# Kernel optimization log

Measured on AMD Instinct MI355X. Metric: run time of the kernel, lower is better.

The kernel has to match this reference:

```python
import jax, jax.numpy as jnp
import numpy as np
from jax import lax

DIM = 256          # C
D_INNER = 512      # expand * dim
D_STATE = 16       # N
DT_RANK = 32       # ceil(d_inner / 16)
K_CONV = 4


def setup_inputs() -> dict:
    key = jax.random.key(0)
    ks = jax.random.split(key, 20)
    B, C, H, W = 2, DIM, 64, 64
    Di, N, R = D_INNER, D_STATE, DT_RANK
    s = 0.02
    inp = {
        "decoder_feat": jax.random.normal(ks[0], (B, C, H, W), jnp.float32),
        "encoder_feat": jax.random.normal(ks[1], (B, C, H, W), jnp.float32),
        # CrossMambaFusion params
        "dec_w": jax.random.normal(ks[2], (C, 2 * Di), jnp.float32) * s,
        "dec_b": jnp.zeros((2 * Di,), jnp.float32),
        "enc_w": jax.random.normal(ks[3], (C, Di), jnp.float32) * s,
        "enc_b": jnp.zeros((Di,), jnp.float32),
        "out_w": jax.random.normal(ks[4], (Di, C), jnp.float32) * s,
        "out_b": jnp.zeros((C,), jnp.float32),
        "ln_g": jnp.ones((C,), jnp.float32),
        "ln_b": jnp.zeros((C,), jnp.float32),
        # Mamba block params (inner dim = Di, expand=1.0)
        "in_w": jax.random.normal(ks[5], (Di, 2 * Di), jnp.float32) * s,
        "in_b": jnp.zeros((2 * Di,), jnp.float32),
        "conv_w": jax.random.normal(ks[6], (Di, 1, K_CONV), jnp.float32) * 0.1,
        "conv_b": jnp.zeros((Di,), jnp.float32),
        "x_proj_w": jax.random.normal(ks[7], (Di, R + 2 * N), jnp.float32) * s,
        "dt_w": jax.random.normal(ks[8], (R, Di), jnp.float32) * 0.1,
        "dt_b": jax.random.uniform(ks[9], (Di,), jnp.float32, -4.0, -2.0),  # small dt after softplus
        "A_log": jnp.log(jnp.tile(jnp.arange(1, N + 1, dtype=jnp.float32)[None, :], (Di, 1))),
        "D_param": jnp.ones((Di,), jnp.float32),
        "m_out_w": jax.random.normal(ks[10], (Di, Di), jnp.float32) * s,
        "m_out_b": jnp.zeros((Di,), jnp.float32),
    }
    return inp


def _mamba(x, in_w, in_b, conv_w, conv_b, x_proj_w, dt_w, dt_b, A_log, D_param, m_out_w, m_out_b):
    # x: (B, L, Di)
    Bsz, L, Di = x.shape
    N, R = D_STATE, DT_RANK
    xz = x @ in_w + in_b                      # (B, L, 2*Di)
    xm, z = jnp.split(xz, 2, axis=-1)
    # causal depthwise conv over the sequence axis
    xc = jnp.swapaxes(xm, 1, 2)               # (B, Di, L)
    xc = lax.conv_general_dilated(
        xc, conv_w, window_strides=(1,), padding=[(K_CONV - 1, 0)],
        dimension_numbers=("NCH", "OIH", "NCH"), feature_group_count=Di)
    xc = xc + conv_b[None, :, None]
    u = jax.nn.silu(jnp.swapaxes(xc, 1, 2))   # (B, L, Di)
    x_dbl = u @ x_proj_w                      # (B, L, R+2N)
    dt = jax.nn.softplus(x_dbl[..., :R] @ dt_w + dt_b)   # (B, L, Di)
    Bm = x_dbl[..., R:R + N]                  # (B, L, N)
    Cm = x_dbl[..., R + N:]                   # (B, L, N)
    A = -jnp.exp(A_log)                       # (Di, N)

    def step(h, t):
        dt_t, u_t, B_t, C_t = t               # (B,Di),(B,Di),(B,N),(B,N)
        dA = jnp.exp(dt_t[..., None] * A)     # (B, Di, N)
        h = h * dA + (dt_t * u_t)[..., None] * B_t[:, None, :]
        y = jnp.einsum("bdn,bn->bd", h, C_t)
        return h, y

    h0 = jnp.zeros((Bsz, Di, N), x.dtype)
    _, ys = lax.scan(step, h0, (jnp.swapaxes(dt, 0, 1), jnp.swapaxes(u, 0, 1),
                                jnp.swapaxes(Bm, 0, 1), jnp.swapaxes(Cm, 0, 1)))
    y = jnp.swapaxes(ys, 0, 1) + u * D_param  # skip connection via D
    y = y * jax.nn.silu(z)
    return y @ m_out_w + m_out_b


def reference(decoder_feat, encoder_feat, dec_w, dec_b, enc_w, enc_b, out_w, out_b,
              ln_g, ln_b, in_w, in_b, conv_w, conv_b, x_proj_w, dt_w, dt_b,
              A_log, D_param, m_out_w, m_out_b):
    B, C, H, W = decoder_feat.shape
    Di = D_INNER
    dec = jnp.transpose(decoder_feat, (0, 2, 3, 1)).reshape(B, H * W, C)
    enc = jnp.transpose(encoder_feat, (0, 2, 3, 1)).reshape(B, H * W, C)
    dec_proj = dec @ dec_w + dec_b
    dec_x, dec_gate = dec_proj[..., :Di], dec_proj[..., Di:]
    enc_p = enc @ enc_w + enc_b
    combined = dec_x * jax.nn.sigmoid(enc_p) + enc_p          # (B, L, Di)
    processed = _mamba(combined, in_w, in_b, conv_w, conv_b, x_proj_w,
                       dt_w, dt_b, A_log, D_param, m_out_w, m_out_b)
    out = (processed * jax.nn.sigmoid(dec_gate)) @ out_w + out_b
    res = out + dec
    mu = jnp.mean(res, axis=-1, keepdims=True)
    var = jnp.mean(jnp.square(res - mu), axis=-1, keepdims=True)
    res = (res - mu) * lax.rsqrt(var + 1e-5) * ln_g + ln_b
    return jnp.transpose(res.reshape(B, H, W, C), (0, 3, 1, 2))
```

## Files before the change

kernel.cpp:

```cpp
#include <hip/hip_runtime.h>
#include <hip/hip_bf16.h>

typedef __bf16 bf16x8_t __attribute__((ext_vector_type(8)));
typedef float f32x4_t __attribute__((ext_vector_type(4)));

__device__ __forceinline__ float sigmoidf_(float x) { return 1.0f / (1.0f + __expf(-x)); }
__device__ __forceinline__ float siluf_(float x) { return x * sigmoidf_(x); }
__device__ __forceinline__ float softplusf_(float x) {
    return fmaxf(x, 0.0f) + log1pf(__expf(-fabsf(x)));
}
__device__ __forceinline__ float b2f(ushort u) { return __uint_as_float(((unsigned)u) << 16); }
__device__ __forceinline__ ushort f2b(float f) {
    return (ushort)__bfloat16_as_ushort(__float2bfloat16(f));
}

__global__ __launch_bounds__(256) void k_prep(
    const float* __restrict__ dec_w, const float* __restrict__ enc_w,
    const float* __restrict__ in_w, const float* __restrict__ m_out_w,
    const float* __restrict__ out_w, const float* __restrict__ x_proj_w,
    const float* __restrict__ dt_w,
    const float* __restrict__ dec, const float* __restrict__ enc,
    __hip_bfloat16* __restrict__ dec_wT, __hip_bfloat16* __restrict__ enc_wT,
    __hip_bfloat16* __restrict__ in_wT, __hip_bfloat16* __restrict__ m_out_wT,
    __hip_bfloat16* __restrict__ out_wT, __hip_bfloat16* __restrict__ xpwT,
    __hip_bfloat16* __restrict__ dtwT,
    __hip_bfloat16* __restrict__ decL, __hip_bfloat16* __restrict__ encL)
{
    __shared__ float tile[64][65];
    if (blockIdx.x < 5312) {
        int gid = blockIdx.x * 256 + threadIdx.x;
        const float* src; __hip_bfloat16* dst; int lk, N, idx;
        if (gid < 262144)       { src = dec_w;    dst = dec_wT;   lk = 8; N = 1024; idx = gid; }
        else if (gid < 393216)  { src = enc_w;    dst = enc_wT;   lk = 8; N = 512;  idx = gid - 262144; }
        else if (gid < 917504)  { src = in_w;     dst = in_wT;    lk = 9; N = 1024; idx = gid - 393216; }
        else if (gid < 1179648) { src = m_out_w;  dst = m_out_wT; lk = 9; N = 512;  idx = gid - 917504; }
        else if (gid < 1310720) { src = out_w;    dst = out_wT;   lk = 9; N = 256;  idx = gid - 1179648; }
        else if (gid < 1343488) { src = x_proj_w; dst = xpwT;     lk = 9; N = 64;   idx = gid - 1310720; }
        else                    { src = dt_w;     dst = dtwT;     lk = 5; N = 512;  idx = gid - 1343488; }
        int K = 1 << lk;
        int n = idx >> lk, k = idx & (K - 1);
        dst[idx] = __float2bfloat16(src[(size_t)k * N + n]);
        return;
    }
    const int bid = blockIdx.x - 5312;
    const int t = threadIdx.x;
    const int ct = bid & 3;
    const int lt = (bid >> 2) & 63;
    const int sel = bid >> 8;
    const int b = sel & 1, ten = sel >> 1;
    const float* src = ten ? enc : dec;
    __hip_bfloat16* dst = ten ? encL : decL;
    const size_t ibase = (size_t)b * 256 * 4096 + (size_t)(ct * 64) * 4096 + (size_t)lt * 64;
#pragma unroll
    for (int i = 0; i < 16; ++i) {
        int c = i * 4 + (t >> 6), l = t & 63;
        tile[c][l] = src[ibase + (size_t)c * 4096 + l];
    }
    __syncthreads();
    const size_t obase = ((size_t)b * 4096 + (size_t)lt * 64) * 256 + ct * 64;
#pragma unroll
    for (int i = 0; i < 16; ++i) {
        int l = i * 4 + (t >> 6), c = t & 63;
        dst[obase + (size_t)l * 256 + c] = __float2bfloat16(tile[c][l]);
    }
}

template <int EPI, int K>
__global__ __launch_bounds__(256) void bgemm(
    const __hip_bfloat16* __restrict__ A, const __hip_bfloat16* __restrict__ Bt,
    const float* __restrict__ bias, void* __restrict__ out0,
    void* __restrict__ out1, const void* __restrict__ extra)
{
    __shared__ ushort At[128 * 32];
    __shared__ ushort Bl[128 * 32];
    const int tid = threadIdx.x;
    const int wave = tid >> 6, lane = tid & 63;
    const int n0 = blockIdx.x * 128, m0 = blockIdx.y * 128;
    const int wm = (wave >> 1) * 64, wn = (wave & 1) * 64;
    f32x4_t acc[4][4] = {};
    const int fr = lane & 15, fq = (lane >> 4) * 8;

    for (int k0 = 0; k0 < K; k0 += 32) {
#pragma unroll
        for (int q = 0; q < 2; ++q) {
            int idx = q * 256 + tid;
            int row = idx >> 2, ch = (idx & 3) * 8;
            uint4 va = *(const uint4*)&A[(size_t)(m0 + row) * K + k0 + ch];
            uint4 vb = *(const uint4*)&Bt[(size_t)(n0 + row) * K + k0 + ch];
            *(uint4*)&At[row * 32 + ch] = va;
            *(uint4*)&Bl[row * 32 + ch] = vb;
        }
        __syncthreads();
        bf16x8_t af[4], bf[4];
#pragma unroll
        for (int i = 0; i < 4; ++i) {
            af[i] = *(bf16x8_t*)&At[(wm + i * 16 + fr) * 32 + fq];
            bf[i] = *(bf16x8_t*)&Bl[(wn + i * 16 + fr) * 32 + fq];
        }
#pragma unroll
        for (int i = 0; i < 4; ++i)
#pragma unroll
            for (int j = 0; j < 4; ++j)
                acc[i][j] = __builtin_amdgcn_mfma_f32_16x16x32_bf16(af[i], bf[j], acc[i][j], 0, 0, 0);
        __syncthreads();
    }

    const int col = lane & 15, rbase = (lane >> 4) * 4;
#pragma unroll
    for (int i = 0; i < 4; ++i) {
#pragma unroll
        for (int j = 0; j < 4; ++j) {
#pragma unroll
            for (int r = 0; r < 4; ++r) {
                int m = m0 + wm + i * 16 + rbase + r;
                int n = n0 + wn + j * 16 + col;
                float v = acc[i][j][r] + bias[n];
                if (EPI == 0) {
                    ((__hip_bfloat16*)out0)[(size_t)m * 512 + n] = __float2bfloat16(v);
                } else if (EPI == 1) {
                    if (n < 512) {
                        float ep = __bfloat162float(((const __hip_bfloat16*)extra)[(size_t)m * 512 + n]);
                        ((__hip_bfloat16*)out0)[(size_t)m * 512 + n] =
                            __float2bfloat16(fmaf(v, sigmoidf_(ep), ep));
                    } else {
                        ((__hip_bfloat16*)out1)[(size_t)m * 512 + (n - 512)] =
                            __float2bfloat16(sigmoidf_(v));
                    }
                } else if (EPI == 2) {
                    if (n < 512)
                        ((__hip_bfloat16*)out0)[(size_t)m * 512 + n] = __float2bfloat16(v);
                    else
                        ((__hip_bfloat16*)out1)[(size_t)m * 512 + (n - 512)] =
                            __float2bfloat16(siluf_(v));
                } else {
                    float g = __bfloat162float(((const __hip_bfloat16*)extra)[(size_t)m * 512 + n]);
                    ((__hip_bfloat16*)out0)[(size_t)m * 512 + n] = __float2bfloat16(v * g);
                }
            }
        }
    }
}

#define CHUNK 16
#define NCHUNK 256

__global__ __launch_bounds__(512) void k_conv_scan(
    const __hip_bfloat16* __restrict__ xm, const float* __restrict__ conv_w,
    const float* __restrict__ conv_b, const __hip_bfloat16* __restrict__ xpwT,
    const __hip_bfloat16* __restrict__ dtwT, const float* __restrict__ dt_b,
    const float* __restrict__ A_log,
    __hip_bfloat16* __restrict__ u_out, float* __restrict__ Bm,
    float* __restrict__ Cm, __hip_bfloat16* __restrict__ dt_out,
    float* __restrict__ hpart, float* __restrict__ dtsums)
{
    __shared__ __align__(16) ushort us_dts[CHUNK][512 + 8];
    __shared__ __align__(16) ushort adt[CHUNK][32 + 8];
    __shared__ float BsL[CHUNK * 16];
    const int tid = threadIdx.x;
    const int wave = tid >> 6, lane = tid & 63;
    const int bl0 = blockIdx.x * CHUNK;
    const int l0 = bl0 & 4095;
    const int b = blockIdx.x >> 8;
    const int chunk = blockIdx.x & (NCHUNK - 1);
    const int fr = lane & 15, fq = (lane >> 4) * 8;
    const int col = lane & 15, rbase = (lane >> 4) * 4;

    float uarr[CHUNK];
    {
        const int d = tid;
        const float cw0 = conv_w[d * 4], cw1 = conv_w[d * 4 + 1];
        const float cw2 = conv_w[d * 4 + 2], cw3 = conv_w[d * 4 + 3];
        const float cb = conv_b[d];
        const ushort* xs = (const ushort*)xm;
        float x0 = (l0 >= 3) ? b2f(xs[(size_t)(bl0 - 3) * 512 + d]) : 0.f;
        float x1 = (l0 >= 2) ? b2f(xs[(size_t)(bl0 - 2) * 512 + d]) : 0.f;
        float x2 = (l0 >= 1) ? b2f(xs[(size_t)(bl0 - 1) * 512 + d]) : 0.f;
#pragma unroll
        for (int t = 0; t < CHUNK; ++t) {
            float x3 = b2f(xs[(size_t)(bl0 + t) * 512 + d]);
            float a = cb;
            a = fmaf(cw0, x0, a);
            a = fmaf(cw1, x1, a);
            a = fmaf(cw2, x2, a);
            a = fmaf(cw3, x3, a);
            float uv = siluf_(a);
            uarr[t] = uv;
            ushort ub = f2b(uv);
            us_dts[t][d] = ub;
            ((ushort*)u_out)[(size_t)(bl0 + t) * 512 + d] = ub;
            x0 = x1; x1 = x2; x2 = x3;
        }
    }
    __syncthreads();

    if (wave < 4) {
        const int n0w = wave * 16;
        f32x4_t acc = {};
        const __hip_bfloat16* bp = xpwT + (size_t)(n0w + fr) * 512;
#pragma unroll
        for (int k0 = 0; k0 < 512; k0 += 32) {
            bf16x8_t af = *(bf16x8_t*)&us_dts[fr][k0 + fq];
            bf16x8_t bf = *(const bf16x8_t*)&bp[k0 + fq];
            acc = __builtin_amdgcn_mfma_f32_16x16x32_bf16(af, bf, acc, 0, 0, 0);
        }
#pragma unroll
        for (int r = 0; r < 4; ++r) {
            int m = rbase + r;
            int n = n0w + col;
            float v = acc[r];
            if (n < 32) {
                adt[m][n] = f2b(v);
            } else if (n < 48) {
                BsL[m * 16 + (n - 32)] = v;
                Bm[(size_t)(bl0 + m) * 16 + (n - 32)] = v;
            } else {
                Cm[(size_t)(bl0 + m) * 16 + (n - 48)] = v;
            }
        }
    }
    __syncthreads();

    {
        bf16x8_t af = *(bf16x8_t*)&adt[fr][fq];
#pragma unroll
        for (int t = 0; t < 4; ++t) {
            int nt = wave * 4 + t;
            bf16x8_t bf = *(const bf16x8_t*)&dtwT[(size_t)(nt * 16 + fr) * 32 + fq];
            f32x4_t acc = {};
            acc = __builtin_amdgcn_mfma_f32_16x16x32_bf16(af, bf, acc, 0, 0, 0);
#pragma unroll
            for (int r = 0; r < 4; ++r) {
                int m = rbase + r;
                int n = nt * 16 + col;
                ushort dv = f2b(softplusf_(acc[r] + dt_b[n]));
                us_dts[m][n] = dv;
                ((ushort*)dt_out)[(size_t)(bl0 + m) * 512 + n] = dv;
            }
        }
    }
    __syncthreads();

    {
        const int d = tid;
        float Av[16];
#pragma unroll
        for (int n = 0; n < 16; n += 4) {
            float4 al = *(const float4*)&A_log[d * 16 + n];
            Av[n + 0] = -__expf(al.x);
            Av[n + 1] = -__expf(al.y);
            Av[n + 2] = -__expf(al.z);
            Av[n + 3] = -__expf(al.w);
        }
        float h[16] = {};
        float dtsum = 0.f;
#pragma unroll
        for (int t = 0; t < CHUNK; ++t) {
            float dtv = b2f(us_dts[t][d]);
            float dtu = dtv * uarr[t];
            dtsum += dtv;
            const float* Bt = &BsL[t * 16];
#pragma unroll
            for (int n = 0; n < 16; ++n)
                h[n] = fmaf(h[n], __expf(dtv * Av[n]), dtu * Bt[n]);
        }
        const size_t sidx = ((size_t)b * NCHUNK + chunk) * 512 + d;
        const size_t idx = sidx * 16;
#pragma unroll
        for (int n = 0; n < 16; n += 4)
            *(float4*)&hpart[idx + n] = make_float4(h[n], h[n + 1], h[n + 2], h[n + 3]);
        dtsums[sidx] = dtsum;
    }
}

__global__ __launch_bounds__(256) void k_scan_comb(
    const float* __restrict__ hpart, const float* __restrict__ dtsums,
    const float* __restrict__ A_log, float* __restrict__ h_in)
{
    const int gid = blockIdx.x * 256 + threadIdx.x;
    const int n = gid & 15;
    const int d = (gid >> 4) & 511;
    const int b = gid >> 13;
    const float Av = -__expf(A_log[d * 16 + n]);
    float h = 0.f;
    for (int c = 0; c < NCHUNK; ++c) {
        const size_t sidx = ((size_t)b * NCHUNK + c) * 512 + d;
        const size_t idx = sidx * 16 + n;
        h_in[idx] = h;
        h = fmaf(h, __expf(Av * dtsums[sidx]), hpart[idx]);
    }
}

__global__ __launch_bounds__(512) void k_scan_fin(
    const __hip_bfloat16* __restrict__ dt, const __hip_bfloat16* __restrict__ u,
    const float* __restrict__ Bmp, const float* __restrict__ Cmp,
    const float* __restrict__ A_log, const float* __restrict__ Dp,
    const __hip_bfloat16* __restrict__ zs, const float* __restrict__ h_in,
    __hip_bfloat16* __restrict__ yout)
{
    __shared__ float Bs[CHUNK * 16];
    __shared__ float Cs[CHUNK * 16];
    const int d = threadIdx.x;
    const int chunk = blockIdx.x & (NCHUNK - 1);
    const int b = blockIdx.x >> 8;
    const size_t row0 = (size_t)b * 4096 + (size_t)chunk * CHUNK;

    if (d < CHUNK * 16) {
        Bs[d] = Bmp[row0 * 16 + d];
        Cs[d] = Cmp[row0 * 16 + d];
    }
    float Av[16];
#pragma unroll
    for (int n = 0; n < 16; n += 4) {
        float4 al = *(const float4*)&A_log[d * 16 + n];
        Av[n + 0] = -__expf(al.x);
        Av[n + 1] = -__expf(al.y);
        Av[n + 2] = -__expf(al.z);
        Av[n + 3] = -__expf(al.w);
    }
    const float Dv = Dp[d];
    float h[16];
    const size_t idx = (((size_t)b * NCHUNK + chunk) * 512 + d) * 16;
#pragma unroll
    for (int n = 0; n < 16; n += 4) {
        float4 hv = *(const float4*)&h_in[idx + n];
        h[n] = hv.x; h[n + 1] = hv.y; h[n + 2] = hv.z; h[n + 3] = hv.w;
    }
    __syncthreads();

    const ushort* dtp = (const ushort*)dt + row0 * 512 + d;
    const ushort* up = (const ushort*)u + row0 * 512 + d;
    const ushort* zp = (const ushort*)zs + row0 * 512 + d;
    __hip_bfloat16* yp = yout + row0 * 512 + d;
#pragma unroll
    for (int t = 0; t < CHUNK; ++t) {
        float dtv = b2f(dtp[(size_t)t * 512]);
        float uv = b2f(up[(size_t)t * 512]);
        float zv = b2f(zp[(size_t)t * 512]);
        float dtu = dtv * uv;
        const float* Bt = &Bs[t * 16];
        const float* Ct = &Cs[t * 16];
        float y = 0.f;
#pragma unroll
        for (int n = 0; n < 16; ++n) {
            h[n] = fmaf(h[n], __expf(dtv * Av[n]), dtu * Bt[n]);
            y = fmaf(h[n], Ct[n], y);
        }
        yp[(size_t)t * 512] = __float2bfloat16((y + uv * Dv) * zv);
    }
}

__global__ __launch_bounds__(256) void k_out_ln(
    const __hip_bfloat16* __restrict__ A, const __hip_bfloat16* __restrict__ Bt,
    const float* __restrict__ bias, const __hip_bfloat16* __restrict__ decL,
    const float* __restrict__ ln_g, const float* __restrict__ ln_b,
    float* __restrict__ outp)
{
    __shared__ ushort At[32 * 32];
    __shared__ ushort Bl[256 * 32];
    __shared__ float red[4][32][2];
    __shared__ float lmu[32], lsc[32];
    const int tid = threadIdx.x;
    const int wave = tid >> 6, lane = tid & 63;
    const int m0 = blockIdx.x * 32;
    const int wn = wave * 64;
    f32x4_t acc[2][4] = {};
    const int fr = lane & 15, fq = (lane >> 4) * 8;

    for (int k0 = 0; k0 < 512; k0 += 32) {
        if (tid < 128) {
            int row = tid >> 2, ch = (tid & 3) * 8;
            *(uint4*)&At[row * 32 + ch] = *(const uint4*)&A[(size_t)(m0 + row) * 512 + k0 + ch];
        }
#pragma unroll
        for (int q = 0; q < 4; ++q) {
            int idx = q * 256 + tid;
            int row = idx >> 2, ch = (idx & 3) * 8;
            *(uint4*)&Bl[row * 32 + ch] = *(const uint4*)&Bt[(size_t)row * 512 + k0 + ch];
        }
        __syncthreads();
        bf16x8_t af[2], bf[4];
#pragma unroll
        for (int i = 0; i < 2; ++i)
            af[i] = *(bf16x8_t*)&At[(i * 16 + fr) * 32 + fq];
#pragma unroll
        for (int j = 0; j < 4; ++j)
            bf[j] = *(bf16x8_t*)&Bl[(wn + j * 16 + fr) * 32 + fq];
#pragma unroll
        for (int i = 0; i < 2; ++i)
#pragma unroll
            for (int j = 0; j < 4; ++j)
                acc[i][j] = __builtin_amdgcn_mfma_f32_16x16x32_bf16(af[i], bf[j], acc[i][j], 0, 0, 0);
        __syncthreads();
    }

    const int col = lane & 15, rbase = (lane >> 4) * 4;
#pragma unroll
    for (int i = 0; i < 2; ++i) {
#pragma unroll
        for (int r = 0; r < 4; ++r) {
            int ml = i * 16 + rbase + r;
            int m = m0 + ml;
            float s = 0.f, sq = 0.f;
#pragma unroll
            for (int j = 0; j < 4; ++j) {
                int n = wn + j * 16 + col;
                float dv = b2f(((const ushort*)decL)[(size_t)m * 256 + n]);
                float v = acc[i][j][r] + bias[n] + dv;
                acc[i][j][r] = v;
                s += v;
                sq = fmaf(v, v, sq);
            }
            s += __shfl_xor(s, 1);  sq += __shfl_xor(sq, 1);
            s += __shfl_xor(s, 2);  sq += __shfl_xor(sq, 2);
            s += __shfl_xor(s, 4);  sq += __shfl_xor(sq, 4);
            s += __shfl_xor(s, 8);  sq += __shfl_xor(sq, 8);
            if (col == 0) { red[wave][ml][0] = s; red[wave][ml][1] = sq; }
        }
    }
    __syncthreads();
    if (tid < 32) {
        float s  = red[0][tid][0] + red[1][tid][0] + red[2][tid][0] + red[3][tid][0];
        float sq = red[0][tid][1] + red[1][tid][1] + red[2][tid][1] + red[3][tid][1];
        float mu = s * (1.0f / 256.0f);
        float var = sq * (1.0f / 256.0f) - mu * mu;
        lmu[tid] = mu;
        lsc[tid] = rsqrtf(var + 1e-5f);
    }
    __syncthreads();
    const int bb = m0 >> 12;
    const int lpos0 = m0 & 4095;
#pragma unroll
    for (int i = 0; i < 2; ++i) {
#pragma unroll
        for (int r = 0; r < 4; ++r) {
            int ml = i * 16 + rbase + r;
            float mu = lmu[ml], sc = lsc[ml];
#pragma unroll
            for (int j = 0; j < 4; ++j) {
                int n = wn + j * 16 + col;
                float v = (acc[i][j][r] - mu) * sc * ln_g[n] + ln_b[n];
                outp[(size_t)bb * (256 * 4096) + (size_t)n * 4096 + lpos0 + ml] = v;
            }
        }
    }
}

extern "C" void kernel_launch(void* const* d_in, const int* in_sizes, int n_in,
                              void* d_out, int out_size, void* d_ws, size_t ws_size,
                              hipStream_t stream)
{
    const float* decoder_feat = (const float*)d_in[0];
    const float* encoder_feat = (const float*)d_in[1];
    const float* dec_w = (const float*)d_in[2];
    const float* dec_b = (const float*)d_in[3];
    const float* enc_w = (const float*)d_in[4];
    const float* enc_b = (const float*)d_in[5];
    const float* out_w = (const float*)d_in[6];
    const float* out_b = (const float*)d_in[7];
    const float* ln_g = (const float*)d_in[8];
    const float* ln_bb = (const float*)d_in[9];
    const float* in_w = (const float*)d_in[10];
    const float* in_b = (const float*)d_in[11];
    const float* conv_w = (const float*)d_in[12];
    const float* conv_b = (const float*)d_in[13];
    const float* x_proj_w = (const float*)d_in[14];
    const float* dt_w = (const float*)d_in[15];
    const float* dt_b = (const float*)d_in[16];
    const float* A_log = (const float*)d_in[17];
    const float* D_param = (const float*)d_in[18];
    const float* m_out_w = (const float*)d_in[19];
    const float* m_out_b = (const float*)d_in[20];

    float* outp = (float*)d_out;
    char* ws = (char*)d_ws;
    const size_t MB = 1024ull * 1024;
    __hip_bfloat16* decL     = (__hip_bfloat16*)(ws + 0 * MB);
    __hip_bfloat16* encL     = (__hip_bfloat16*)(ws + 4 * MB);
    __hip_bfloat16* dec_wT   = (__hip_bfloat16*)(ws + 8 * MB);
    __hip_bfloat16* enc_wT   = (__hip_bfloat16*)(ws + 9 * MB);
    __hip_bfloat16* in_wT    = (__hip_bfloat16*)(ws + 10 * MB);
    __hip_bfloat16* m_out_wT = (__hip_bfloat16*)(ws + 11 * MB);
    __hip_bfloat16* out_wT   = (__hip_bfloat16*)(ws + 12 * MB);
    __hip_bfloat16* xpwT     = (__hip_bfloat16*)(ws + 12 * MB + 262144);
    __hip_bfloat16* dtwT     = (__hip_bfloat16*)(ws + 12 * MB + 262144 + 65536);
    __hip_bfloat16* enc_pb   = (__hip_bfloat16*)(ws + 13 * MB);
    __hip_bfloat16* combined = (__hip_bfloat16*)(ws + 29 * MB);
    __hip_bfloat16* gate_sig = (__hip_bfloat16*)(ws + 37 * MB);
    __hip_bfloat16* xm       = (__hip_bfloat16*)(ws + 45 * MB);
    __hip_bfloat16* z_silu   = (__hip_bfloat16*)(ws + 53 * MB);
    __hip_bfloat16* u_buf    = (__hip_bfloat16*)(ws + 61 * MB);
    __hip_bfloat16* dt_buf   = (__hip_bfloat16*)(ws + 69 * MB);
    float* h_in              = (float*)(ws + 77 * MB);
    float* Bm                = (float*)(ws + 93 * MB);
    float* Cm                = (float*)(ws + 93 * MB + 524288);
    float* dtsums            = (float*)(ws + 94 * MB);
    float* hpart = (float*)(ws + 13 * MB);
    __hip_bfloat16* y_buf = combined;
    __hip_bfloat16* gated = xm;

    k_prep<<<6336, 256, 0, stream>>>(
        dec_w, enc_w, in_w, m_out_w, out_w, x_proj_w, dt_w,
        decoder_feat, encoder_feat,
        dec_wT, enc_wT, in_wT, m_out_wT, out_wT, xpwT, dtwT, decL, encL);
    bgemm<0, 256><<<dim3(4, 64), 256, 0, stream>>>(
        encL, enc_wT, enc_b, enc_pb, nullptr, nullptr);
    bgemm<1, 256><<<dim3(8, 64), 256, 0, stream>>>(
        decL, dec_wT, dec_b, combined, gate_sig, enc_pb);
    bgemm<2, 512><<<dim3(8, 64), 256, 0, stream>>>(
        combined, in_wT, in_b, xm, z_silu, nullptr);
    k_conv_scan<<<2 * NCHUNK, 512, 0, stream>>>(
        xm, conv_w, conv_b, xpwT, dtwT, dt_b, A_log,
        u_buf, Bm, Cm, dt_buf, hpart, dtsums);
    k_scan_comb<<<64, 256, 0, stream>>>(hpart, dtsums, A_log, h_in);
    k_scan_fin<<<2 * NCHUNK, 512, 0, stream>>>(
        dt_buf, u_buf, Bm, Cm, A_log, D_param, z_silu, h_in, y_buf);
    bgemm<3, 512><<<dim3(4, 64), 256, 0, stream>>>(
        y_buf, m_out_wT, m_out_b, gated, nullptr, gate_sig);
    k_out_ln<<<256, 256, 0, stream>>>(
        gated, out_wT, out_b, decL, ln_g, ln_bb, outp);
}
```

Baseline: 279.7 us.

## Fuse enc/dec projections, fuse m_out GEMM with out-proj+LN, batch scan combine loads

Merges the encoder and decoder projection GEMMs into one kernel that keeps the encoder result in registers, so the enc_p intermediate is never written to or read back from memory. The Mamba output projection and gating are folded into the final out-projection/LayerNorm kernel, with the gated tile held in shared memory. This removes the gated buffer round trip and one launch. The scan-combine kernel now issues 16 chunk loads at a time to hide latency, with more smaller blocks. In exchange the fused m_out stage recomputes with only 256 blocks of 32 rows and reloads the full 512x512 weight per block, which may lower parallelism.

```diff
diff --git a/kernel.cpp b/kernel.cpp
--- a/kernel.cpp
+++ b/kernel.cpp
@@ -117,15 +117,6 @@
                 float v = acc[i][j][r] + bias[n];
                 if (EPI == 0) {
                     ((__hip_bfloat16*)out0)[(size_t)m * 512 + n] = __float2bfloat16(v);
-                } else if (EPI == 1) {
-                    if (n < 512) {
-                        float ep = __bfloat162float(((const __hip_bfloat16*)extra)[(size_t)m * 512 + n]);
-                        ((__hip_bfloat16*)out0)[(size_t)m * 512 + n] =
-                            __float2bfloat16(fmaf(v, sigmoidf_(ep), ep));
-                    } else {
-                        ((__hip_bfloat16*)out1)[(size_t)m * 512 + (n - 512)] =
-                            __float2bfloat16(sigmoidf_(v));
-                    }
                 } else if (EPI == 2) {
                     if (n < 512)
                         ((__hip_bfloat16*)out0)[(size_t)m * 512 + n] = __float2bfloat16(v);
@@ -138,6 +129,101 @@
                 }
             }
         }
+    }
+}
+
+__global__ __launch_bounds__(256) void k_dec_enc(
+    const __hip_bfloat16* __restrict__ decL, const __hip_bfloat16* __restrict__ encL,
+    const __hip_bfloat16* __restrict__ dec_wT, const __hip_bfloat16* __restrict__ enc_wT,
+    const float* __restrict__ dec_b, const float* __restrict__ enc_b,
+    __hip_bfloat16* __restrict__ combined, __hip_bfloat16* __restrict__ gate_sig)
+{
+    __shared__ __align__(16) ushort At[128 * 32];
+    __shared__ __align__(16) ushort Bl[128 * 32];
+    const int tid = threadIdx.x;
+    const int wave = tid >> 6, lane = tid & 63;
+    const int n0 = blockIdx.x * 128, m0 = blockIdx.y * 128;
+    const int wm = (wave >> 1) * 64, wn = (wave & 1) * 64;
+    const int fr = lane & 15, fq = (lane >> 4) * 8;
+    const int col = lane & 15, rbase = (lane >> 4) * 4;
+
+    f32x4_t accD[4][4] = {};
+    for (int k0 = 0; k0 < 256; k0 += 32) {
+#pragma unroll
+        for (int q = 0; q < 2; ++q) {
+            int idx = q * 256 + tid;
+            int row = idx >> 2, ch = (idx & 3) * 8;
+            uint4 va = *(const uint4*)&decL[(size_t)(m0 + row) * 256 + k0 + ch];
+            uint4 vb = *(const uint4*)&dec_wT[(size_t)(n0 + row) * 256 + k0 + ch];
+            *(uint4*)&At[row * 32 + ch] = va;
+            *(uint4*)&Bl[row * 32 + ch] = vb;
+        }
+        __syncthreads();
+        bf16x8_t af[4], bf[4];
+#pragma unroll
+        for (int i = 0; i < 4; ++i) {
+            af[i] = *(bf16x8_t*)&At[(wm + i * 16 + fr) * 32 + fq];
+            bf[i] = *(bf16x8_t*)&Bl[(wn + i * 16 + fr) * 32 + fq];
+        }
+#pragma unroll
+        for (int i = 0; i < 4; ++i)
+#pragma unroll
+            for (int j = 0; j < 4; ++j)
+                accD[i][j] = __builtin_amdgcn_mfma_f32_16x16x32_bf16(af[i], bf[j], accD[i][j], 0, 0, 0);
+        __syncthreads();
+    }
+
+    if (n0 < 512) {
+        f32x4_t accE[4][4] = {};
+        for (int k0 = 0; k0 < 256; k0 += 32) {
+#pragma unroll
+            for (int q = 0; q < 2; ++q) {
+                int idx = q * 256 + tid;
+                int row = idx >> 2, ch = (idx & 3) * 8;
+                uint4 va = *(const uint4*)&encL[(size_t)(m0 + row) * 256 + k0 + ch];
+                uint4 vb = *(const uint4*)&enc_wT[(size_t)(n0 + row) * 256 + k0 + ch];
+                *(uint4*)&At[row * 32 + ch] = va;
+                *(uint4*)&Bl[row * 32 + ch] = vb;
+            }
+            __syncthreads();
+            bf16x8_t af[4], bf[4];
+#pragma unroll
+            for (int i = 0; i < 4; ++i) {
+                af[i] = *(bf16x8_t*)&At[(wm + i * 16 + fr) * 32 + fq];
+                bf[i] = *(bf16x8_t*)&Bl[(wn + i * 16 + fr) * 32 + fq];
+            }
+#pragma unroll
+            for (int i = 0; i < 4; ++i)
+#pragma unroll
+                for (int j = 0; j < 4; ++j)
+                    accE[i][j] = __builtin_amdgcn_mfma_f32_16x16x32_bf16(af[i], bf[j], accE[i][j], 0, 0, 0);
+            __syncthreads();
+        }
+#pragma unroll
+        for (int i = 0; i < 4; ++i)
+#pragma unroll
+            for (int j = 0; j < 4; ++j)
+#pragma unroll
+                for (int r = 0; r < 4; ++r) {
+                    int m = m0 + wm + i * 16 + rbase + r;
+                    int n = n0 + wn + j * 16 + col;
+                    float ep = accE[i][j][r] + enc_b[n];
+                    float v = accD[i][j][r] + dec_b[n];
+                    combined[(size_t)m * 512 + n] =
+                        __float2bfloat16(fmaf(v, sigmoidf_(ep), ep));
+                }
+    } else {
+#pragma unroll
+        for (int i = 0; i < 4; ++i)
+#pragma unroll
+            for (int j = 0; j < 4; ++j)
+#pragma unroll
+                for (int r = 0; r < 4; ++r) {
+                    int m = m0 + wm + i * 16 + rbase + r;
+                    int n = n0 + wn + j * 16 + col;
+                    float v = accD[i][j][r] + dec_b[n];
+                    gate_sig[(size_t)m * 512 + (n - 512)] = __float2bfloat16(sigmoidf_(v));
+                }
     }
 }
 
@@ -272,21 +358,34 @@
     }
 }
 
-__global__ __launch_bounds__(256) void k_scan_comb(
+__global__ __launch_bounds__(128) void k_scan_comb(
     const float* __restrict__ hpart, const float* __restrict__ dtsums,
     const float* __restrict__ A_log, float* __restrict__ h_in)
 {
-    const int gid = blockIdx.x * 256 + threadIdx.x;
+    const int gid = blockIdx.x * 128 + threadIdx.x;
     const int n = gid & 15;
     const int d = (gid >> 4) & 511;
     const int b = gid >> 13;
     const float Av = -__expf(A_log[d * 16 + n]);
+    const size_t base = (size_t)b * NCHUNK;
     float h = 0.f;
-    for (int c = 0; c < NCHUNK; ++c) {
-        const size_t sidx = ((size_t)b * NCHUNK + c) * 512 + d;
-        const size_t idx = sidx * 16 + n;
-        h_in[idx] = h;
-        h = fmaf(h, __expf(Av * dtsums[sidx]), hpart[idx]);
+    for (int c0 = 0; c0 < NCHUNK; c0 += 16) {
+        float hp[16], ef[16];
+#pragma unroll
+        for (int u = 0; u < 16; ++u) {
+            const size_t sidx = (base + c0 + u) * 512 + d;
+            hp[u] = hpart[sidx * 16 + n];
+            ef[u] = dtsums[sidx];
+        }
+#pragma unroll
+        for (int u = 0; u < 16; ++u)
+            ef[u] = __expf(Av * ef[u]);
+#pragma unroll
+        for (int u = 0; u < 16; ++u) {
+            const size_t sidx = (base + c0 + u) * 512 + d;
+            h_in[sidx * 16 + n] = h;
+            h = fmaf(h, ef[u], hp[u]);
+        }
     }
 }
 
@@ -349,51 +448,98 @@
     }
 }
 
-__global__ __launch_bounds__(256) void k_out_ln(
-    const __hip_bfloat16* __restrict__ A, const __hip_bfloat16* __restrict__ Bt,
-    const float* __restrict__ bias, const __hip_bfloat16* __restrict__ decL,
+__global__ __launch_bounds__(256) void k_mout_ln(
+    const __hip_bfloat16* __restrict__ Y, const __hip_bfloat16* __restrict__ mwT,
+    const float* __restrict__ m_out_b, const __hip_bfloat16* __restrict__ gate,
+    const __hip_bfloat16* __restrict__ owT, const float* __restrict__ out_b,
+    const __hip_bfloat16* __restrict__ decL,
     const float* __restrict__ ln_g, const float* __restrict__ ln_b,
     float* __restrict__ outp)
 {
-    __shared__ ushort At[32 * 32];
-    __shared__ ushort Bl[256 * 32];
+    __shared__ __align__(16) ushort Gs[32][520];
+    __shared__ __align__(16) ushort At[32 * 32];
+    __shared__ __align__(16) ushort Bl[512 * 32];
     __shared__ float red[4][32][2];
     __shared__ float lmu[32], lsc[32];
     const int tid = threadIdx.x;
     const int wave = tid >> 6, lane = tid & 63;
     const int m0 = blockIdx.x * 32;
-    const int wn = wave * 64;
-    f32x4_t acc[2][4] = {};
     const int fr = lane & 15, fq = (lane >> 4) * 8;
-
+    const int col = lane & 15, rbase = (lane >> 4) * 4;
+
+#pragma unroll
+    for (int q = 0; q < 8; ++q) {
+        int idx = q * 256 + tid;
+        int row = idx >> 6, ch = (idx & 63) * 8;
+        *(uint4*)&Gs[row][ch] = *(const uint4*)&gate[(size_t)(m0 + row) * 512 + ch];
+    }
+
+    const int wn1 = wave * 128;
+    f32x4_t acc1[2][8] = {};
     for (int k0 = 0; k0 < 512; k0 += 32) {
         if (tid < 128) {
             int row = tid >> 2, ch = (tid & 3) * 8;
-            *(uint4*)&At[row * 32 + ch] = *(const uint4*)&A[(size_t)(m0 + row) * 512 + k0 + ch];
-        }
+            *(uint4*)&At[row * 32 + ch] = *(const uint4*)&Y[(size_t)(m0 + row) * 512 + k0 + ch];
+        }
+#pragma unroll
+        for (int q = 0; q < 8; ++q) {
+            int idx = q * 256 + tid;
+            int row = idx >> 2, ch = (idx & 3) * 8;
+            *(uint4*)&Bl[row * 32 + ch] = *(const uint4*)&mwT[(size_t)row * 512 + k0 + ch];
+        }
+        __syncthreads();
+        bf16x8_t af[2], bf[8];
+#pragma unroll
+        for (int i = 0; i < 2; ++i)
+            af[i] = *(bf16x8_t*)&At[(i * 16 + fr) * 32 + fq];
+#pragma unroll
+        for (int j = 0; j < 8; ++j)
+            bf[j] = *(bf16x8_t*)&Bl[(wn1 + j * 16 + fr) * 32 + fq];
+#pragma unroll
+        for (int i = 0; i < 2; ++i)
+#pragma unroll
+            for (int j = 0; j < 8; ++j)
+                acc1[i][j] = __builtin_amdgcn_mfma_f32_16x16x32_bf16(af[i], bf[j], acc1[i][j], 0, 0, 0);
+        __syncthreads();
+    }
+#pragma unroll
+    for (int i = 0; i < 2; ++i)
+#pragma unroll
+        for (int j = 0; j < 8; ++j)
+#pragma unroll
+            for (int r = 0; r < 4; ++r) {
+                int m = i * 16 + rbase + r;
+                int n = wn1 + j * 16 + col;
+                float g = b2f(Gs[m][n]);
+                Gs[m][n] = f2b((acc1[i][j][r] + m_out_b[n]) * g);
+            }
+    __syncthreads();
+
+    const int wn2 = wave * 64;
+    f32x4_t acc2[2][4] = {};
+    for (int k0 = 0; k0 < 512; k0 += 32) {
 #pragma unroll
         for (int q = 0; q < 4; ++q) {
             int idx = q * 256 + tid;
             int row = idx >> 2, ch = (idx & 3) * 8;
-            *(uint4*)&Bl[row * 32 + ch] = *(const uint4*)&Bt[(size_t)row * 512 + k0 + ch];
+            *(uint4*)&Bl[row * 32 + ch] = *(const uint4*)&owT[(size_t)row * 512 + k0 + ch];
         }
         __syncthreads();
         bf16x8_t af[2], bf[4];
 #pragma unroll
         for (int i = 0; i < 2; ++i)
-            af[i] = *(bf16x8_t*)&At[(i * 16 + fr) * 32 + fq];
+            af[i] = *(bf16x8_t*)&Gs[i * 16 + fr][k0 + fq];
 #pragma unroll
         for (int j = 0; j < 4; ++j)
-            bf[j] = *(bf16x8_t*)&Bl[(wn + j * 16 + fr) * 32 + fq];
+            bf[j] = *(bf16x8_t*)&Bl[(wn2 + j * 16 + fr) * 32 + fq];
 #pragma unroll
         for (int i = 0; i < 2; ++i)
 #pragma unroll
             for (int j = 0; j < 4; ++j)
-                acc[i][j] = __builtin_amdgcn_mfma_f32_16x16x32_bf16(af[i], bf[j], acc[i][j], 0, 0, 0);
-        __syncthreads();
-    }
-
-    const int col = lane & 15, rbase = (lane >> 4) * 4;
+                acc2[i][j] = __builtin_amdgcn_mfma_f32_16x16x32_bf16(af[i], bf[j], acc2[i][j], 0, 0, 0);
+        __syncthreads();
+    }
+
 #pragma unroll
     for (int i = 0; i < 2; ++i) {
 #pragma unroll
@@ -403,10 +549,10 @@
             float s = 0.f, sq = 0.f;
 #pragma unroll
             for (int j = 0; j < 4; ++j) {
-                int n = wn + j * 16 + col;
+                int n = wn2 + j * 16 + col;
                 float dv = b2f(((const ushort*)decL)[(size_t)m * 256 + n]);
-                float v = acc[i][j][r] + bias[n] + dv;
-                acc[i][j][r] = v;
+                float v = acc2[i][j][r] + out_b[n] + dv;
+                acc2[i][j][r] = v;
                 s += v;
                 sq = fmaf(v, v, sq);
             }
@@ -437,8 +583,8 @@
             float mu = lmu[ml], sc = lsc[ml];
 #pragma unroll
             for (int j = 0; j < 4; ++j) {
-                int n = wn + j * 16 + col;
-                float v = (acc[i][j][r] - mu) * sc * ln_g[n] + ln_b[n];
+                int n = wn2 + j * 16 + col;
+                float v = (acc2[i][j][r] - mu) * sc * ln_g[n] + ln_b[n];
                 outp[(size_t)bb * (256 * 4096) + (size_t)n * 4096 + lpos0 + ml] = v;
             }
         }
@@ -483,7 +629,6 @@
     __hip_bfloat16* out_wT   = (__hip_bfloat16*)(ws + 12 * MB);
     __hip_bfloat16* xpwT     = (__hip_bfloat16*)(ws + 12 * MB + 262144);
     __hip_bfloat16* dtwT     = (__hip_bfloat16*)(ws + 12 * MB + 262144 + 65536);
-    __hip_bfloat16* enc_pb   = (__hip_bfloat16*)(ws + 13 * MB);
     __hip_bfloat16* combined = (__hip_bfloat16*)(ws + 29 * MB);
     __hip_bfloat16* gate_sig = (__hip_bfloat16*)(ws + 37 * MB);
     __hip_bfloat16* xm       = (__hip_bfloat16*)(ws + 45 * MB);
@@ -496,26 +641,21 @@
     float* dtsums            = (float*)(ws + 94 * MB);
     float* hpart = (float*)(ws + 13 * MB);
     __hip_bfloat16* y_buf = combined;
-    __hip_bfloat16* gated = xm;
 
     k_prep<<<6336, 256, 0, stream>>>(
         dec_w, enc_w, in_w, m_out_w, out_w, x_proj_w, dt_w,
         decoder_feat, encoder_feat,
         dec_wT, enc_wT, in_wT, m_out_wT, out_wT, xpwT, dtwT, decL, encL);
-    bgemm<0, 256><<<dim3(4, 64), 256, 0, stream>>>(
-        encL, enc_wT, enc_b, enc_pb, nullptr, nullptr);
-    bgemm<1, 256><<<dim3(8, 64), 256, 0, stream>>>(
-        decL, dec_wT, dec_b, combined, gate_sig, enc_pb);
+    k_dec_enc<<<dim3(8, 64), 256, 0, stream>>>(
+        decL, encL, dec_wT, enc_wT, dec_b, enc_b, combined, gate_sig);
     bgemm<2, 512><<<dim3(8, 64), 256, 0, stream>>>(
         combined, in_wT, in_b, xm, z_silu, nullptr);
     k_conv_scan<<<2 * NCHUNK, 512, 0, stream>>>(
         xm, conv_w, conv_b, xpwT, dtwT, dt_b, A_log,
         u_buf, Bm, Cm, dt_buf, hpart, dtsums);
-    k_scan_comb<<<64, 256, 0, stream>>>(hpart, dtsums, A_log, h_in);
+    k_scan_comb<<<128, 128, 0, stream>>>(hpart, dtsums, A_log, h_in);
     k_scan_fin<<<2 * NCHUNK, 512, 0, stream>>>(
         dt_buf, u_buf, Bm, Cm, A_log, D_param, z_silu, h_in, y_buf);
-    bgemm<3, 512><<<dim3(4, 64), 256, 0, stream>>>(
-        y_buf, m_out_wT, m_out_b, gated, nullptr, gate_sig);
-    k_out_ln<<<256, 256, 0, stream>>>(
-        gated, out_wT, out_b, decL, ln_g, ln_bb, outp);
-}
+    k_mout_ln<<<256, 256, 0, stream>>>(
+        y_buf, m_out_wT, m_out_b, gate_sig, out_wT, out_b, decL, ln_g, ln_bb, outp);
+}
```

New measurement: 264.9 us. -5.3%, faster.
